# Kernel optimization log

Hardware: AMD Instinct MI355X
Metric: run time of the kernel (lower is better)

The kernel has to match this reference:

```python
import math
import jax, jax.numpy as jnp
import numpy as np

B, L, D, H, DFF = 2, 2048, 1024, 16, 4096
HD = D // H
NUM_BUCKETS, MAX_DISTANCE = 32, 128


def setup_inputs() -> dict:
    key = jax.random.key(0)
    ks = jax.random.split(key, 10)
    s = 0.02
    return {
        "hidden_states": jax.random.normal(ks[0], (B, L, D), dtype=jnp.float32),
        "Wq": jax.random.normal(ks[1], (D, D), dtype=jnp.float32) * s,
        "Wk": jax.random.normal(ks[2], (D, D), dtype=jnp.float32) * s,
        "Wv": jax.random.normal(ks[3], (D, D), dtype=jnp.float32) * s,
        "Wo": jax.random.normal(ks[4], (D, D), dtype=jnp.float32) * s,
        "W1": jax.random.normal(ks[5], (D, DFF), dtype=jnp.float32) * s,
        "W2": jax.random.normal(ks[6], (DFF, D), dtype=jnp.float32) * s,
        "ln1_g": jnp.ones((D,), dtype=jnp.float32),
        "ln2_g": jnp.ones((D,), dtype=jnp.float32),
        "rel_table": jax.random.normal(ks[7], (NUM_BUCKETS, H), dtype=jnp.float32) * s,
    }


def rms_norm(x, g, eps=1e-6):
    # T5-style LayerNorm: scale only, no mean subtraction
    var = jnp.mean(jnp.square(x.astype(jnp.float32)), axis=-1, keepdims=True)
    return (x.astype(jnp.float32) * jax.lax.rsqrt(var + eps)).astype(x.dtype) * g


def relative_position_bias(seq_len, table):
    # bidirectional T5 bucket scheme, num_buckets=32, max_distance=128
    ctx = jnp.arange(seq_len)[:, None]
    mem = jnp.arange(seq_len)[None, :]
    rp = mem - ctx                                  # (L, L) int
    nb = NUM_BUCKETS // 2
    buckets = (rp > 0).astype(jnp.int32) * nb
    rpa = jnp.abs(rp)
    max_exact = nb // 2
    is_small = rpa < max_exact
    safe = jnp.maximum(rpa, 1).astype(jnp.float32)  # avoid log(0); masked by is_small
    large = max_exact + (
        jnp.log(safe / max_exact) / math.log(MAX_DISTANCE / max_exact) * (nb - max_exact)
    ).astype(jnp.int32)
    large = jnp.minimum(large, nb - 1)
    buckets = buckets + jnp.where(is_small, rpa, large)   # (L, L)
    vals = table[buckets]                                  # (L, L, H)
    return jnp.transpose(vals, (2, 0, 1))[None]            # (1, H, L, L)


def reference(hidden_states, Wq, Wk, Wv, Wo, W1, W2, ln1_g, ln2_g, rel_table):
    x = hidden_states
    b, l, d = x.shape

    # --- self-attention sublayer (pre-norm) ---
    h = rms_norm(x, ln1_g)
    q = (h @ Wq).reshape(b, l, H, HD)
    k = (h @ Wk).reshape(b, l, H, HD)
    v = (h @ Wv).reshape(b, l, H, HD)

    bias = relative_position_bias(l, rel_table)            # (1, H, L, L)
    # NOTE: source's manual attention path has NO 1/sqrt(head_dim) scaling
    scores = jnp.einsum("bqhd,bkhd->bhqk", q, k) + bias
    attn = jax.nn.softmax(scores.astype(jnp.float32), axis=-1).astype(scores.dtype)
    out = jnp.einsum("bhqk,bkhd->bqhd", attn, v).reshape(b, l, d)
    x = x + out @ Wo

    # --- feed-forward sublayer (pre-norm) ---
    h = rms_norm(x, ln2_g)
    x = x + jax.nn.relu(h @ W1) @ W2
    return x
```

## Files before the change

### kernel.cpp

```cpp
#include <hip/hip_runtime.h>
#include <hip/hip_bf16.h>
#include <math.h>

#define BDIM 1024
#define HEADS 16
#define HDIM 64
#define LSEQ 2048
#define NBATCH 2
#define DFFDIM 4096
#define QKVN 3072

typedef __bf16 bf16x8_t __attribute__((ext_vector_type(8)));
typedef float f32x4_t __attribute__((ext_vector_type(4)));

__device__ __forceinline__ ushort f2bf(float f) {
    union { __hip_bfloat16 b; ushort u; } cv;
    cv.b = __float2bfloat16(f);
    return cv.u;
}
__device__ __forceinline__ float bf2f(ushort u) {
    union { unsigned int i; float f; } cv;
    cv.i = ((unsigned int)u) << 16;
    return cv.f;
}

__global__ __launch_bounds__(256) void transpose_cvt(const float* __restrict__ W,
                                                     ushort* __restrict__ Wt,
                                                     int K, int N) {
    __shared__ ushort tile[32][33];
    int bi = blockIdx.y;
    int bj = blockIdx.x;
    int tx = threadIdx.x;
    int ty = threadIdx.y;
#pragma unroll
    for (int r = 0; r < 4; ++r) {
        int krow = bi * 32 + ty + r * 8;
        int ncol = bj * 32 + tx;
        tile[ty + r * 8][tx] = f2bf(W[(size_t)krow * N + ncol]);
    }
    __syncthreads();
#pragma unroll
    for (int r = 0; r < 4; ++r) {
        int nrow = bj * 32 + ty + r * 8;
        int kcol = bi * 32 + tx;
        Wt[(size_t)nrow * K + kcol] = tile[tx][ty + r * 8];
    }
}

__global__ __launch_bounds__(256) void transpose_cvt4(const float* __restrict__ W0,
                                                      const float* __restrict__ W1,
                                                      const float* __restrict__ W2,
                                                      const float* __restrict__ W3,
                                                      ushort* __restrict__ T0,
                                                      ushort* __restrict__ T1,
                                                      ushort* __restrict__ T2,
                                                      ushort* __restrict__ T3) {
    __shared__ ushort tile[32][33];
    const int z = blockIdx.z;
    const float* W = z == 0 ? W0 : z == 1 ? W1 : z == 2 ? W2 : W3;
    ushort* T = z == 0 ? T0 : z == 1 ? T1 : z == 2 ? T2 : T3;
    int bi = blockIdx.y, bj = blockIdx.x;
    int tx = threadIdx.x, ty = threadIdx.y;
#pragma unroll
    for (int r = 0; r < 4; ++r)
        tile[ty + r * 8][tx] = f2bf(W[(size_t)(bi * 32 + ty + r * 8) * 1024 + bj * 32 + tx]);
    __syncthreads();
#pragma unroll
    for (int r = 0; r < 4; ++r)
        T[(size_t)(bj * 32 + ty + r * 8) * 1024 + bi * 32 + tx] = tile[tx][ty + r * 8];
}

__global__ __launch_bounds__(256) void rmsnorm_k(const float* __restrict__ x,
                                                 const float* __restrict__ g,
                                                 ushort* __restrict__ out) {
    int row = blockIdx.x;
    int t = threadIdx.x;
    int w = t >> 6, l = t & 63;
    const float4 v = reinterpret_cast<const float4*>(x + (size_t)row * BDIM)[t];
    float ss = v.x * v.x + v.y * v.y + v.z * v.z + v.w * v.w;
#pragma unroll
    for (int m = 1; m <= 32; m <<= 1) ss += __shfl_xor(ss, m);
    __shared__ float wsum[4];
    if (l == 0) wsum[w] = ss;
    __syncthreads();
    float tot = wsum[0] + wsum[1] + wsum[2] + wsum[3];
    float r = rsqrtf(tot * (1.0f / BDIM) + 1e-6f);
    const float4 gv = reinterpret_cast<const float4*>(g)[t];
    ushort4 o;
    o.x = f2bf(v.x * r * gv.x);
    o.y = f2bf(v.y * r * gv.y);
    o.z = f2bf(v.z * r * gv.z);
    o.w = f2bf(v.w * r * gv.w);
    reinterpret_cast<ushort4*>(out + (size_t)row * BDIM)[t] = o;
}

__global__ void bias_table_k(const float* __restrict__ rel, float* __restrict__ btab) {
    int idx = blockIdx.x * 256 + threadIdx.x;
    if (idx >= HEADS * 4095) return;
    int h = idx / 4095;
    int d = idx % 4095;
    int rp = d - 2047;
    int bucket = rp > 0 ? 16 : 0;
    int rpa = rp < 0 ? -rp : rp;
    if (rpa < 8) {
        bucket += rpa;
    } else {
        int large = 8 + (int)(logf((float)rpa * 0.125f) * (1.0f / logf(16.0f)) * 8.0f);
        bucket += large < 15 ? large : 15;
    }
    btab[idx] = rel[bucket * HEADS + h];
}

__global__ __launch_bounds__(256) void reduce2_k(const ushort* __restrict__ parts,
                                                 const float* __restrict__ res,
                                                 float* __restrict__ out,
                                                 size_t mn) {
    size_t i = ((size_t)blockIdx.x * 256 + threadIdx.x) * 4;
    float4 r = *(const float4*)(res + i);
    ushort4 a = *(const ushort4*)(parts + i);
    ushort4 b = *(const ushort4*)(parts + mn + i);
    float4 o;
    o.x = r.x + bf2f(a.x) + bf2f(b.x);
    o.y = r.y + bf2f(a.y) + bf2f(b.y);
    o.z = r.z + bf2f(a.z) + bf2f(b.z);
    o.w = r.w + bf2f(a.w) + bf2f(b.w);
    *(float4*)(out + i) = o;
}

__global__ __launch_bounds__(256) void reduce2_rms(const ushort* __restrict__ parts,
                                                   const float* __restrict__ res,
                                                   const float* __restrict__ g,
                                                   float* __restrict__ out,
                                                   ushort* __restrict__ hout,
                                                   size_t mn) {
    int row = blockIdx.x;
    int t = threadIdx.x;
    int w = t >> 6, l = t & 63;
    size_t i = (size_t)row * BDIM + t * 4;
    float4 r = *(const float4*)(res + i);
    ushort4 a = *(const ushort4*)(parts + i);
    ushort4 b = *(const ushort4*)(parts + mn + i);
    float4 o;
    o.x = r.x + bf2f(a.x) + bf2f(b.x);
    o.y = r.y + bf2f(a.y) + bf2f(b.y);
    o.z = r.z + bf2f(a.z) + bf2f(b.z);
    o.w = r.w + bf2f(a.w) + bf2f(b.w);
    *(float4*)(out + i) = o;
    float ss = o.x * o.x + o.y * o.y + o.z * o.z + o.w * o.w;
#pragma unroll
    for (int m = 1; m <= 32; m <<= 1) ss += __shfl_xor(ss, m);
    __shared__ float wsum[4];
    if (l == 0) wsum[w] = ss;
    __syncthreads();
    float tot = wsum[0] + wsum[1] + wsum[2] + wsum[3];
    float rr = rsqrtf(tot * (1.0f / BDIM) + 1e-6f);
    const float4 gv = reinterpret_cast<const float4*>(g)[t];
    ushort4 h;
    h.x = f2bf(o.x * rr * gv.x);
    h.y = f2bf(o.y * rr * gv.y);
    h.z = f2bf(o.z * rr * gv.z);
    h.w = f2bf(o.w * rr * gv.w);
    reinterpret_cast<ushort4*>(hout + (size_t)row * BDIM)[t] = h;
}

template <int MODE, int TM, int TN>
__global__ __launch_bounds__(256) void gemm_bt(const ushort* __restrict__ A,
                                               const ushort* __restrict__ Bt,
                                               void* Cout, const float* res,
                                               ushort* __restrict__ vtb,
                                               int M, int N, int K, int nbx, int nkc) {
    __shared__ __align__(16) ushort As[TM * 64];
    __shared__ __align__(16) ushort Bs[TN * 64];
    constexpr int MF = TM / 32, NF = TN / 32;
    const int nwg = gridDim.x;
    const int bid = blockIdx.x;
    const int swz = (bid & 7) * (nwg >> 3) + (bid >> 3);
    const int nxy = nwg / nkc;
    const int chunk = swz / nxy;
    const int bxy = swz % nxy;
    const int bx = bxy % nbx, by = bxy / nbx;
    const int Kc = K / nkc;
    const int kbeg = chunk * Kc;
    const int tid = threadIdx.x;
    const int w = tid >> 6, l = tid & 63;
    const int wm = w >> 1, wn = w & 1;
    const int rowA0 = by * TM;
    const int colB0 = bx * TN;
    const int lr = l >> 3;
    const int scs = ((l & 7) ^ lr) * 8;
    const int c = l & 15, gq = l >> 4;
    const int rswz = (c & 7) * 8;
    f32x4_t acc[MF][NF] = {};

    auto stage = [&](int k0) {
#pragma unroll
        for (int i = 0; i < TM / 32; ++i) {
            int r = i * 32 + w * 8;
            __builtin_amdgcn_global_load_lds(
                (const __attribute__((address_space(1))) uint32_t*)(A + (size_t)(rowA0 + r + lr) * K + kbeg + k0 + scs),
                (__attribute__((address_space(3))) uint32_t*)(&As[r * 64]), 16, 0, 0);
        }
#pragma unroll
        for (int i = 0; i < TN / 32; ++i) {
            int r = i * 32 + w * 8;
            __builtin_amdgcn_global_load_lds(
                (const __attribute__((address_space(1))) uint32_t*)(Bt + (size_t)(colB0 + r + lr) * K + kbeg + k0 + scs),
                (__attribute__((address_space(3))) uint32_t*)(&Bs[r * 64]), 16, 0, 0);
        }
    };

    const int nk = Kc >> 6;
    for (int kt = 0; kt < nk; ++kt) {
        __syncthreads();
        stage(kt << 6);
        __syncthreads();
#pragma unroll
        for (int kk = 0; kk < 2; ++kk) {
            bf16x8_t av[MF], bv[NF];
#pragma unroll
            for (int mf = 0; mf < MF; ++mf)
                av[mf] = *(const bf16x8_t*)&As[(wm * (TM / 2) + mf * 16 + c) * 64 + ((kk * 32 + gq * 8) ^ rswz)];
#pragma unroll
            for (int nf = 0; nf < NF; ++nf)
                bv[nf] = *(const bf16x8_t*)&Bs[(wn * (TN / 2) + nf * 16 + c) * 64 + ((kk * 32 + gq * 8) ^ rswz)];
#pragma unroll
            for (int mf = 0; mf < MF; ++mf)
#pragma unroll
                for (int nf = 0; nf < NF; ++nf)
                    acc[mf][nf] = __builtin_amdgcn_mfma_f32_16x16x32_bf16(av[mf], bv[nf], acc[mf][nf], 0, 0, 0);
        }
    }
    if (MODE == 4 && colB0 >= 2048) {
#pragma unroll
        for (int mf = 0; mf < MF; ++mf) {
#pragma unroll
            for (int nf = 0; nf < NF; ++nf) {
                int col = colB0 + wn * (TN / 2) + nf * 16 + c;
                int v = col - 2048;
                int hh = v >> 6, hd = v & 63;
                int row0 = rowA0 + wm * (TM / 2) + mf * 16 + gq * 4;
                int bb = row0 >> 11, key = row0 & 2047;
                ushort4 ov;
                ov.x = f2bf(acc[mf][nf][0]);
                ov.y = f2bf(acc[mf][nf][1]);
                ov.z = f2bf(acc[mf][nf][2]);
                ov.w = f2bf(acc[mf][nf][3]);
                *(ushort4*)(vtb + ((size_t)((bb * 16 + hh) * 64 + hd)) * 2048 + key) = ov;
            }
        }
        return;
    }
#pragma unroll
    for (int mf = 0; mf < MF; ++mf) {
#pragma unroll
        for (int nf = 0; nf < NF; ++nf) {
#pragma unroll
            for (int i = 0; i < 4; ++i) {
                int row = rowA0 + wm * (TM / 2) + mf * 16 + gq * 4 + i;
                int col = colB0 + wn * (TN / 2) + nf * 16 + c;
                size_t idx = (size_t)row * N + col;
                float vv = acc[mf][nf][i];
                if (MODE == 0 || MODE == 4) {
                    ((ushort*)Cout)[idx] = f2bf(vv);
                } else if (MODE == 1) {
                    ((float*)Cout)[idx] = res[idx] + vv;
                } else if (MODE == 2) {
                    ((ushort*)Cout)[idx] = f2bf(vv > 0.f ? vv : 0.f);
                } else {
                    ((ushort*)Cout)[(size_t)chunk * M * N + idx] = f2bf(vv);
                }
            }
        }
    }
}

template <int MODE>
__global__ __launch_bounds__(512, 1) void gemm_bt8(const ushort* __restrict__ A,
                                                   const ushort* __restrict__ Bt,
                                                   void* Cout,
                                                   int M, int N, int K, int nbx) {
    __shared__ __align__(16) ushort As[2][256 * 64];
    __shared__ __align__(16) ushort Bs[2][256 * 64];
    const int nwg = gridDim.x;
    const int bid = blockIdx.x;
    const int swz = (bid & 7) * (nwg >> 3) + (bid >> 3);
    const int bx = swz % nbx, by = swz / nbx;
    const int tid = threadIdx.x;
    const int w = tid >> 6, l = tid & 63;
    const int wm = w >> 2, wn = w & 3;
    const int rowA0 = by * 256, colB0 = bx * 256;
    const int st_r = tid >> 3;
    const int scs = ((l & 7) ^ (st_r & 7)) * 8;
    const int c = l & 15, gq = l >> 4;
    const int rswz = (c & 7) * 8;
    f32x4_t acc[8][4] = {};

    auto stageChunk = [&](int buf, int k0, int q) {
        __builtin_amdgcn_global_load_lds(
            (const __attribute__((address_space(1))) uint32_t*)(A + (size_t)(rowA0 + q * 64 + st_r) * K + k0 + scs),
            (__attribute__((address_space(3))) uint32_t*)(&As[buf][(q * 64 + w * 8) * 64]), 16, 0, 0);
        __builtin_amdgcn_global_load_lds(
            (const __attribute__((address_space(1))) uint32_t*)(Bt + (size_t)(colB0 + q * 64 + st_r) * K + k0 + scs),
            (__attribute__((address_space(3))) uint32_t*)(&Bs[buf][(q * 64 + w * 8) * 64]), 16, 0, 0);
    };

    const int nk = K >> 6;
    stageChunk(0, 0, 0);
    stageChunk(0, 0, 1);
    stageChunk(0, 0, 2);
    stageChunk(0, 0, 3);
    asm volatile("s_waitcnt vmcnt(0)" ::: "memory");
    __builtin_amdgcn_s_barrier();
    __builtin_amdgcn_sched_barrier(0);

    for (int k = 0; k < nk; ++k) {
        const int cur = k & 1;
        const ushort* Ab = &As[cur][0];
        const ushort* Bb = &Bs[cur][0];
#pragma unroll
        for (int q = 0; q < 4; ++q) {
            const int mh = q >> 1, nh = q & 1;
            bf16x8_t av[4][2], bv[2][2];
#pragma unroll
            for (int mf = 0; mf < 4; ++mf)
#pragma unroll
                for (int kk = 0; kk < 2; ++kk)
                    av[mf][kk] = *(const bf16x8_t*)&Ab[(wm * 128 + mh * 64 + mf * 16 + c) * 64 + ((kk * 32 + gq * 8) ^ rswz)];
#pragma unroll
            for (int nf = 0; nf < 2; ++nf)
#pragma unroll
                for (int kk = 0; kk < 2; ++kk)
                    bv[nf][kk] = *(const bf16x8_t*)&Bb[(wn * 64 + nh * 32 + nf * 16 + c) * 64 + ((kk * 32 + gq * 8) ^ rswz)];
            if (k + 1 < nk) {
                if (q == 0) { stageChunk(cur ^ 1, (k + 1) << 6, 0); stageChunk(cur ^ 1, (k + 1) << 6, 1); }
                else if (q == 1) { stageChunk(cur ^ 1, (k + 1) << 6, 2); stageChunk(cur ^ 1, (k + 1) << 6, 3); }
            }
            __builtin_amdgcn_s_barrier();
            __builtin_amdgcn_sched_barrier(0);
            __builtin_amdgcn_s_setprio(1);
#pragma unroll
            for (int kk = 0; kk < 2; ++kk)
#pragma unroll
                for (int mf = 0; mf < 4; ++mf)
#pragma unroll
                    for (int nf = 0; nf < 2; ++nf)
                        acc[mh * 4 + mf][nh * 2 + nf] = __builtin_amdgcn_mfma_f32_16x16x32_bf16(
                            av[mf][kk], bv[nf][kk], acc[mh * 4 + mf][nh * 2 + nf], 0, 0, 0);
            __builtin_amdgcn_s_setprio(0);
            if (q == 3 && k + 1 < nk)
                asm volatile("s_waitcnt vmcnt(0)" ::: "memory");
            __builtin_amdgcn_s_barrier();
            __builtin_amdgcn_sched_barrier(0);
        }
    }
#pragma unroll
    for (int am = 0; am < 8; ++am) {
#pragma unroll
        for (int an = 0; an < 4; ++an) {
#pragma unroll
            for (int i = 0; i < 4; ++i) {
                int row = rowA0 + wm * 128 + am * 16 + gq * 4 + i;
                int col = colB0 + wn * 64 + an * 16 + c;
                size_t idx = (size_t)row * N + col;
                float vv = acc[am][an][i];
                if (MODE == 2) {
                    ((ushort*)Cout)[idx] = f2bf(vv > 0.f ? vv : 0.f);
                } else {
                    ((ushort*)Cout)[idx] = f2bf(vv);
                }
            }
        }
    }
}

__global__ __launch_bounds__(512) void attn_fwd(const ushort* __restrict__ qkv,
                                                const ushort* __restrict__ vT,
                                                const float* __restrict__ btab,
                                                ushort* __restrict__ ob) {
    const int tid = threadIdx.x, w = tid >> 6, l = tid & 63;
    const int bh = blockIdx.y, b = bh >> 4, h = bh & 15;
    const int qt = blockIdx.x;
    __shared__ __align__(16) ushort Ks[2][64 * 64];
    __shared__ __align__(16) ushort Vs[2][64 * 64];
    __shared__ __align__(16) ushort Pl[8][16 * 72];
    const int q0 = qt * 128 + w * 16;
    const int c = l & 15, g = l >> 4;
    const size_t rowbase = (size_t)b * LSEQ * QKVN;
    const ushort* qp = qkv + rowbase + h * HDIM;
    const ushort* kp = qkv + rowbase + BDIM + h * HDIM;
    const ushort* vtp = vT + (size_t)bh * HDIM * LSEQ;
    const int sr = tid >> 3;
    const int scs = ((l & 7) ^ (l >> 3)) * 8;
    const float* btq4 = btab + h * 4095 + 2047 - (q0 + c) + g * 4;

    bf16x8_t aq[2];
#pragma unroll
    for (int kk = 0; kk < 2; ++kk)
        aq[kk] = *(const bf16x8_t*)(qp + (size_t)(q0 + c) * QKVN + kk * 32 + g * 8);

    float lrow = 0.f;
    f32x4_t o[4] = {};
    f32x4_t s[4];

    auto stage = [&](int buf, int key0) {
        __builtin_amdgcn_global_load_lds(
            (const __attribute__((address_space(1))) uint32_t*)(kp + (size_t)(key0 + sr) * QKVN + scs),
            (__attribute__((address_space(3))) uint32_t*)(&Ks[buf][(w * 8) * 64]), 16, 0, 0);
        __builtin_amdgcn_global_load_lds(
            (const __attribute__((address_space(1))) uint32_t*)(vtp + (size_t)sr * LSEQ + key0 + scs),
            (__attribute__((address_space(3))) uint32_t*)(&Vs[buf][(w * 8) * 64]), 16, 0, 0);
    };
    auto loadBias = [&](int key0) {
#pragma unroll
        for (int nf = 0; nf < 4; ++nf)
#pragma unroll
            for (int i = 0; i < 4; ++i)
                s[nf][i] = btq4[key0 + nf * 16 + i];
    };

    stage(0, 0);
    loadBias(0);
    int cur = 0;

    ushort* Pw = Pl[w];
    const int rswz = (c & 7) << 3;
    for (int kt = 0; kt < 32; ++kt) {
        __syncthreads();
        if (kt < 31) stage(cur ^ 1, kt * 64 + 64);
#pragma unroll
        for (int kk = 0; kk < 2; ++kk)
#pragma unroll
            for (int nf = 0; nf < 4; ++nf) {
                bf16x8_t kf = *(const bf16x8_t*)&Ks[cur][(nf * 16 + c) * 64 + ((kk * 32 + g * 8) ^ rswz)];
                s[nf] = __builtin_amdgcn_mfma_f32_16x16x32_bf16(kf, aq[kk], s[nf], 0, 0, 0);
            }
        float rs = 0.f;
        union { ushort us[4]; uint2 u2; } pk[4];
#pragma unroll
        for (int nf = 0; nf < 4; ++nf)
#pragma unroll
            for (int i = 0; i < 4; ++i) {
                float pv = __expf(s[nf][i]);
                rs += pv;
                pk[nf].us[i] = f2bf(pv);
            }
        if (kt < 31) loadBias(kt * 64 + 64);
        lrow += rs;
#pragma unroll
        for (int nf = 0; nf < 4; ++nf)
            *(uint2*)&Pw[c * 72 + nf * 16 + g * 4] = pk[nf].u2;
        bf16x8_t pa[2];
#pragma unroll
        for (int kk = 0; kk < 2; ++kk)
            pa[kk] = *(const bf16x8_t*)&Pw[c * 72 + kk * 32 + g * 8];
#pragma unroll
        for (int kk = 0; kk < 2; ++kk)
#pragma unroll
            for (int hf = 0; hf < 4; ++hf) {
                bf16x8_t vf = *(const bf16x8_t*)&Vs[cur][(hf * 16 + c) * 64 + ((kk * 32 + g * 8) ^ rswz)];
                o[hf] = __builtin_amdgcn_mfma_f32_16x16x32_bf16(vf, pa[kk], o[hf], 0, 0, 0);
            }
        cur ^= 1;
    }
    lrow += __shfl_xor(lrow, 16);
    lrow += __shfl_xor(lrow, 32);
    const float inv = 1.f / lrow;
    ushort* orow = ob + (size_t)(b * LSEQ + q0 + c) * BDIM + h * HDIM + g * 4;
#pragma unroll
    for (int hf = 0; hf < 4; ++hf) {
        ushort4 ov;
        ov.x = f2bf(o[hf][0] * inv);
        ov.y = f2bf(o[hf][1] * inv);
        ov.z = f2bf(o[hf][2] * inv);
        ov.w = f2bf(o[hf][3] * inv);
        *(ushort4*)(orow + hf * 16) = ov;
    }
}

extern "C" void kernel_launch(void* const* d_in, const int* in_sizes, int n_in,
                              void* d_out, int out_size, void* d_ws, size_t ws_size,
                              hipStream_t stream) {
    const float* x   = (const float*)d_in[0];
    const float* Wq  = (const float*)d_in[1];
    const float* Wk  = (const float*)d_in[2];
    const float* Wv  = (const float*)d_in[3];
    const float* Wo  = (const float*)d_in[4];
    const float* W1  = (const float*)d_in[5];
    const float* W2  = (const float*)d_in[6];
    const float* g1  = (const float*)d_in[7];
    const float* g2  = (const float*)d_in[8];
    const float* rel = (const float*)d_in[9];
    float* out = (float*)d_out;

    char* ws = (char*)d_ws;
    const size_t MB = 1024 * 1024;
    ushort* wqkvT = (ushort*)(ws + 0 * MB);
    ushort* woT   = (ushort*)(ws + 6 * MB);
    ushort* w1T   = (ushort*)(ws + 8 * MB);
    ushort* w2T   = (ushort*)(ws + 16 * MB);
    float*  btab  = (float*)(ws + 24 * MB);
    ushort* hbuf  = (ushort*)(ws + 25 * MB);
    ushort* qkvb  = (ushort*)(ws + 33 * MB);
    ushort* woP   = (ushort*)(ws + 33 * MB);
    ushort* f1b   = (ushort*)(ws + 33 * MB);
    ushort* vTb   = (ushort*)(ws + 57 * MB);
    ushort* w2P   = (ushort*)(ws + 0 * MB);
    (void)in_sizes; (void)n_in; (void)out_size; (void)ws_size;

    const size_t MN = (size_t)4096 * 1024;
    dim3 tb(32, 8);
    transpose_cvt4<<<dim3(32, 32, 4), tb, 0, stream>>>(Wq, Wk, Wv, Wo,
        wqkvT, wqkvT + 1024 * 1024, wqkvT + 2048 * 1024, woT);
    transpose_cvt<<<dim3(128, 32), tb, 0, stream>>>(W1, w1T, 1024, 4096);
    transpose_cvt<<<dim3(32, 128), tb, 0, stream>>>(W2, w2T, 4096, 1024);
    bias_table_k<<<256, 256, 0, stream>>>(rel, btab);

    rmsnorm_k<<<4096, 256, 0, stream>>>(x, g1, hbuf);
    gemm_bt<4, 128, 128><<<768, 256, 0, stream>>>(hbuf, wqkvT, qkvb, nullptr, vTb, 4096, QKVN, 1024, 24, 1);
    attn_fwd<<<dim3(16, 32), 512, 0, stream>>>(qkvb, vTb, btab, hbuf);
    gemm_bt<3, 128, 128><<<512, 256, 0, stream>>>(hbuf, woT, woP, nullptr, nullptr, 4096, 1024, 1024, 8, 2);
    reduce2_rms<<<4096, 256, 0, stream>>>(woP, x, g2, out, hbuf, MN);
    gemm_bt8<2><<<256, 512, 0, stream>>>(hbuf, w1T, f1b, 4096, DFFDIM, 1024, 16);
    gemm_bt<3, 128, 128><<<512, 256, 0, stream>>>(f1b, w2T, w2P, nullptr, nullptr, 4096, 1024, 4096, 8, 2);
    reduce2_k<<<4096, 256, 0, stream>>>(w2P, out, out, MN);
}
```

Baseline: 226.1 us.

## Move QKV and W2 GEMMs to 256x256 pipelined kernel with 4-way split-K

The QKV projection, including its transposed-V epilogue, moves from the 128x128 gemm_bt kernel to the 256x256 double-buffered gemm_bt8 kernel. The W2 GEMM also uses gemm_bt8, with 4-way split-K instead of 2-way, writing four bf16 partials that a new reduce4 kernel sums with the residual. The larger tiles are meant to raise data reuse and MFMA efficiency. In exchange, the QKV grid shrinks to 192 blocks, which may underfill the GPU, and the extra partial buffers add memory traffic in the final reduction.

```diff
diff --git a/kernel.cpp b/kernel.cpp
--- a/kernel.cpp
+++ b/kernel.cpp
@@ -109,22 +109,6 @@
         bucket += large < 15 ? large : 15;
     }
     btab[idx] = rel[bucket * HEADS + h];
-}
-
-__global__ __launch_bounds__(256) void reduce2_k(const ushort* __restrict__ parts,
-                                                 const float* __restrict__ res,
-                                                 float* __restrict__ out,
-                                                 size_t mn) {
-    size_t i = ((size_t)blockIdx.x * 256 + threadIdx.x) * 4;
-    float4 r = *(const float4*)(res + i);
-    ushort4 a = *(const ushort4*)(parts + i);
-    ushort4 b = *(const ushort4*)(parts + mn + i);
-    float4 o;
-    o.x = r.x + bf2f(a.x) + bf2f(b.x);
-    o.y = r.y + bf2f(a.y) + bf2f(b.y);
-    o.z = r.z + bf2f(a.z) + bf2f(b.z);
-    o.w = r.w + bf2f(a.w) + bf2f(b.w);
-    *(float4*)(out + i) = o;
 }
 
 __global__ __launch_bounds__(256) void reduce2_rms(const ushort* __restrict__ parts,
@@ -163,11 +147,29 @@
     reinterpret_cast<ushort4*>(hout + (size_t)row * BDIM)[t] = h;
 }
 
+__global__ __launch_bounds__(256) void reduce4_k(const ushort* __restrict__ p01,
+                                                 const ushort* __restrict__ p23,
+                                                 const float* __restrict__ res,
+                                                 float* __restrict__ out,
+                                                 size_t mn) {
+    size_t i = ((size_t)blockIdx.x * 256 + threadIdx.x) * 4;
+    float4 r = *(const float4*)(res + i);
+    ushort4 a = *(const ushort4*)(p01 + i);
+    ushort4 b = *(const ushort4*)(p01 + mn + i);
+    ushort4 c = *(const ushort4*)(p23 + i);
+    ushort4 d = *(const ushort4*)(p23 + mn + i);
+    float4 o;
+    o.x = r.x + bf2f(a.x) + bf2f(b.x) + bf2f(c.x) + bf2f(d.x);
+    o.y = r.y + bf2f(a.y) + bf2f(b.y) + bf2f(c.y) + bf2f(d.y);
+    o.z = r.z + bf2f(a.z) + bf2f(b.z) + bf2f(c.z) + bf2f(d.z);
+    o.w = r.w + bf2f(a.w) + bf2f(b.w) + bf2f(c.w) + bf2f(d.w);
+    *(float4*)(out + i) = o;
+}
+
 template <int MODE, int TM, int TN>
 __global__ __launch_bounds__(256) void gemm_bt(const ushort* __restrict__ A,
                                                const ushort* __restrict__ Bt,
-                                               void* Cout, const float* res,
-                                               ushort* __restrict__ vtb,
+                                               void* Cout,
                                                int M, int N, int K, int nbx, int nkc) {
     __shared__ __align__(16) ushort As[TM * 64];
     __shared__ __align__(16) ushort Bs[TN * 64];
@@ -230,26 +232,6 @@
                     acc[mf][nf] = __builtin_amdgcn_mfma_f32_16x16x32_bf16(av[mf], bv[nf], acc[mf][nf], 0, 0, 0);
         }
     }
-    if (MODE == 4 && colB0 >= 2048) {
-#pragma unroll
-        for (int mf = 0; mf < MF; ++mf) {
-#pragma unroll
-            for (int nf = 0; nf < NF; ++nf) {
-                int col = colB0 + wn * (TN / 2) + nf * 16 + c;
-                int v = col - 2048;
-                int hh = v >> 6, hd = v & 63;
-                int row0 = rowA0 + wm * (TM / 2) + mf * 16 + gq * 4;
-                int bb = row0 >> 11, key = row0 & 2047;
-                ushort4 ov;
-                ov.x = f2bf(acc[mf][nf][0]);
-                ov.y = f2bf(acc[mf][nf][1]);
-                ov.z = f2bf(acc[mf][nf][2]);
-                ov.w = f2bf(acc[mf][nf][3]);
-                *(ushort4*)(vtb + ((size_t)((bb * 16 + hh) * 64 + hd)) * 2048 + key) = ov;
-            }
-        }
-        return;
-    }
 #pragma unroll
     for (int mf = 0; mf < MF; ++mf) {
 #pragma unroll
@@ -259,16 +241,7 @@
                 int row = rowA0 + wm * (TM / 2) + mf * 16 + gq * 4 + i;
                 int col = colB0 + wn * (TN / 2) + nf * 16 + c;
                 size_t idx = (size_t)row * N + col;
-                float vv = acc[mf][nf][i];
-                if (MODE == 0 || MODE == 4) {
-                    ((ushort*)Cout)[idx] = f2bf(vv);
-                } else if (MODE == 1) {
-                    ((float*)Cout)[idx] = res[idx] + vv;
-                } else if (MODE == 2) {
-                    ((ushort*)Cout)[idx] = f2bf(vv > 0.f ? vv : 0.f);
-                } else {
-                    ((ushort*)Cout)[(size_t)chunk * M * N + idx] = f2bf(vv);
-                }
+                ((ushort*)Cout)[(size_t)chunk * M * N + idx] = f2bf(acc[mf][nf][i]);
             }
         }
     }
@@ -277,14 +250,20 @@
 template <int MODE>
 __global__ __launch_bounds__(512, 1) void gemm_bt8(const ushort* __restrict__ A,
                                                    const ushort* __restrict__ Bt,
-                                                   void* Cout,
-                                                   int M, int N, int K, int nbx) {
+                                                   void* Cout, void* Cout2,
+                                                   ushort* __restrict__ vtb,
+                                                   int M, int N, int K, int nbx, int nkc) {
     __shared__ __align__(16) ushort As[2][256 * 64];
     __shared__ __align__(16) ushort Bs[2][256 * 64];
     const int nwg = gridDim.x;
     const int bid = blockIdx.x;
     const int swz = (bid & 7) * (nwg >> 3) + (bid >> 3);
-    const int bx = swz % nbx, by = swz / nbx;
+    const int nxy = nwg / nkc;
+    const int chunk = swz / nxy;
+    const int bxy = swz % nxy;
+    const int bx = bxy % nbx, by = bxy / nbx;
+    const int Kc = K / nkc;
+    const int kbeg = chunk * Kc;
     const int tid = threadIdx.x;
     const int w = tid >> 6, l = tid & 63;
     const int wm = w >> 2, wn = w & 3;
@@ -297,14 +276,14 @@
 
     auto stageChunk = [&](int buf, int k0, int q) {
         __builtin_amdgcn_global_load_lds(
-            (const __attribute__((address_space(1))) uint32_t*)(A + (size_t)(rowA0 + q * 64 + st_r) * K + k0 + scs),
+            (const __attribute__((address_space(1))) uint32_t*)(A + (size_t)(rowA0 + q * 64 + st_r) * K + kbeg + k0 + scs),
             (__attribute__((address_space(3))) uint32_t*)(&As[buf][(q * 64 + w * 8) * 64]), 16, 0, 0);
         __builtin_amdgcn_global_load_lds(
-            (const __attribute__((address_space(1))) uint32_t*)(Bt + (size_t)(colB0 + q * 64 + st_r) * K + k0 + scs),
+            (const __attribute__((address_space(1))) uint32_t*)(Bt + (size_t)(colB0 + q * 64 + st_r) * K + kbeg + k0 + scs),
             (__attribute__((address_space(3))) uint32_t*)(&Bs[buf][(q * 64 + w * 8) * 64]), 16, 0, 0);
     };
 
-    const int nk = K >> 6;
+    const int nk = Kc >> 6;
     stageChunk(0, 0, 0);
     stageChunk(0, 0, 1);
     stageChunk(0, 0, 2);
@@ -353,6 +332,31 @@
             __builtin_amdgcn_sched_barrier(0);
         }
     }
+    if (MODE == 4 && colB0 >= 2048) {
+#pragma unroll
+        for (int am = 0; am < 8; ++am) {
+#pragma unroll
+            for (int an = 0; an < 4; ++an) {
+                int col = colB0 + wn * 64 + an * 16 + c;
+                int v = col - 2048;
+                int hh = v >> 6, hd = v & 63;
+                int row0 = rowA0 + wm * 128 + am * 16 + gq * 4;
+                int bb = row0 >> 11, key = row0 & 2047;
+                ushort4 ov;
+                ov.x = f2bf(acc[am][an][0]);
+                ov.y = f2bf(acc[am][an][1]);
+                ov.z = f2bf(acc[am][an][2]);
+                ov.w = f2bf(acc[am][an][3]);
+                *(ushort4*)(vtb + ((size_t)((bb * 16 + hh) * 64 + hd)) * 2048 + key) = ov;
+            }
+        }
+        return;
+    }
+    ushort* dst;
+    if (MODE == 3)
+        dst = (ushort*)(chunk < 2 ? Cout : Cout2) + (size_t)(chunk & 1) * M * N;
+    else
+        dst = (ushort*)Cout;
 #pragma unroll
     for (int am = 0; am < 8; ++am) {
 #pragma unroll
@@ -364,9 +368,9 @@
                 size_t idx = (size_t)row * N + col;
                 float vv = acc[am][an][i];
                 if (MODE == 2) {
-                    ((ushort*)Cout)[idx] = f2bf(vv > 0.f ? vv : 0.f);
+                    dst[idx] = f2bf(vv > 0.f ? vv : 0.f);
                 } else {
-                    ((ushort*)Cout)[idx] = f2bf(vv);
+                    dst[idx] = f2bf(vv);
                 }
             }
         }
@@ -504,7 +508,8 @@
     ushort* woP   = (ushort*)(ws + 33 * MB);
     ushort* f1b   = (ushort*)(ws + 33 * MB);
     ushort* vTb   = (ushort*)(ws + 57 * MB);
-    ushort* w2P   = (ushort*)(ws + 0 * MB);
+    ushort* w2P0  = (ushort*)(ws + 0 * MB);
+    ushort* w2P1  = (ushort*)(ws + 65 * MB);
     (void)in_sizes; (void)n_in; (void)out_size; (void)ws_size;
 
     const size_t MN = (size_t)4096 * 1024;
@@ -516,11 +521,11 @@
     bias_table_k<<<256, 256, 0, stream>>>(rel, btab);
 
     rmsnorm_k<<<4096, 256, 0, stream>>>(x, g1, hbuf);
-    gemm_bt<4, 128, 128><<<768, 256, 0, stream>>>(hbuf, wqkvT, qkvb, nullptr, vTb, 4096, QKVN, 1024, 24, 1);
+    gemm_bt8<4><<<192, 512, 0, stream>>>(hbuf, wqkvT, qkvb, nullptr, vTb, 4096, QKVN, 1024, 12, 1);
     attn_fwd<<<dim3(16, 32), 512, 0, stream>>>(qkvb, vTb, btab, hbuf);
-    gemm_bt<3, 128, 128><<<512, 256, 0, stream>>>(hbuf, woT, woP, nullptr, nullptr, 4096, 1024, 1024, 8, 2);
+    gemm_bt<3, 128, 128><<<512, 256, 0, stream>>>(hbuf, woT, woP, 4096, 1024, 1024, 8, 2);
     reduce2_rms<<<4096, 256, 0, stream>>>(woP, x, g2, out, hbuf, MN);
-    gemm_bt8<2><<<256, 512, 0, stream>>>(hbuf, w1T, f1b, 4096, DFFDIM, 1024, 16);
-    gemm_bt<3, 128, 128><<<512, 256, 0, stream>>>(f1b, w2T, w2P, nullptr, nullptr, 4096, 1024, 4096, 8, 2);
-    reduce2_k<<<4096, 256, 0, stream>>>(w2P, out, out, MN);
-}
+    gemm_bt8<2><<<256, 512, 0, stream>>>(hbuf, w1T, f1b, nullptr, nullptr, 4096, DFFDIM, 1024, 16, 1);
+    gemm_bt8<3><<<256, 512, 0, stream>>>(f1b, w2T, w2P0, w2P1, nullptr, 4096, 1024, 4096, 4, 4);
+    reduce4_k<<<4096, 256, 0, stream>>>(w2P0, w2P1, out, out, MN);
+}
```

New measurement: 238.1 us. +5.3%, slower.
